# Kernel optimization log

Measured on AMD Instinct MI355X. Metric: run time of the kernel, lower is better.

Reference implementation:

```python
import jax, jax.numpy as jnp
import numpy as np

S, B, E, D, H, F, L = 1024, 8, 768, 8, 8, 2048, 4
D = 1024  # HIDDEN_DIM
H = 8     # nhead
DH = D // H
EPS = 1e-5


def _ln(x, g, b):
    m = jnp.mean(x, -1, keepdims=True)
    v = jnp.mean(jnp.square(x - m), -1, keepdims=True)
    return (x - m) * jax.lax.rsqrt(v + EPS) * g + b


def setup_inputs() -> dict:
    key = jax.random.key(0)
    ks = iter(jax.random.split(key, 16))
    n = lambda shape: jax.random.normal(next(ks), shape, jnp.float32) * 0.02
    return dict(
        x=jax.random.normal(next(ks), (S, B, E), jnp.float32),
        enc_w=n((D, E)), enc_b=jnp.zeros((D,), jnp.float32),
        enc_ln_g=jnp.ones((D,), jnp.float32), enc_ln_b=jnp.zeros((D,), jnp.float32),
        qkv_w=n((L, 3 * D, D)), qkv_b=jnp.zeros((L, 3 * D), jnp.float32),
        out_w=n((L, D, D)), out_b=jnp.zeros((L, D), jnp.float32),
        ln1_g=jnp.ones((L, D), jnp.float32), ln1_b=jnp.zeros((L, D), jnp.float32),
        ff1_w=n((L, F, D)), ff1_b=jnp.zeros((L, F), jnp.float32),
        ff2_w=n((L, D, F)), ff2_b=jnp.zeros((L, D), jnp.float32),
        ln2_g=jnp.ones((L, D), jnp.float32), ln2_b=jnp.zeros((L, D), jnp.float32),
        dec_w1=n((D // 2, D)), dec_b1=jnp.zeros((D // 2,), jnp.float32),
        dec_ln_g=jnp.ones((D // 2,), jnp.float32), dec_ln_b=jnp.zeros((D // 2,), jnp.float32),
        dec_w2=n((E, D // 2)), dec_b2=jnp.zeros((E,), jnp.float32),
    )


def reference(x, enc_w, enc_b, enc_ln_g, enc_ln_b, qkv_w, qkv_b, out_w, out_b,
              ln1_g, ln1_b, ff1_w, ff1_b, ff2_w, ff2_b, ln2_g, ln2_b,
              dec_w1, dec_b1, dec_ln_g, dec_ln_b, dec_w2, dec_b2):
    # encoder MLP: Linear -> LayerNorm -> ReLU (dropout = identity at eval)
    h = jax.nn.relu(_ln(x @ enc_w.T + enc_b, enc_ln_g, enc_ln_b))  # (S,B,D)
    scale = np.float32(1.0 / np.sqrt(DH))
    for l in range(L):  # 4 post-norm TransformerEncoderLayers, eager attention
        qkv = h @ qkv_w[l].T + qkv_b[l]                    # (S,B,3D)
        q, k, v = jnp.split(qkv, 3, axis=-1)
        q = q.reshape(S, B, H, DH)
        k = k.reshape(S, B, H, DH)
        v = v.reshape(S, B, H, DH)
        scores = jnp.einsum('sbhd,tbhd->bhst', q, k) * scale  # (B,H,S,S)
        p = jax.nn.softmax(scores, axis=-1)
        o = jnp.einsum('bhst,tbhd->sbhd', p, v).reshape(S, B, D)
        o = o @ out_w[l].T + out_b[l]
        h = _ln(h + o, ln1_g[l], ln1_b[l])
        f = jax.nn.relu(h @ ff1_w[l].T + ff1_b[l]) @ ff2_w[l].T + ff2_b[l]
        h = _ln(h + f, ln2_g[l], ln2_b[l])
    # decoder MLP
    d = jax.nn.relu(_ln(h @ dec_w1.T + dec_b1, dec_ln_g, dec_ln_b))
    return d @ dec_w2.T + dec_b2  # (S,B,E)
```

## Files before the change

kernel.cpp:

```cpp
#include <hip/hip_runtime.h>
#include <math.h>

#define S_ 1024
#define B_ 8
#define E_ 768
#define D_ 1024
#define H_ 8
#define F_ 2048
#define L_ 4
#define M_ (S_*B_)

typedef unsigned short u16;
typedef unsigned int u32;
typedef u16 u16x8 __attribute__((ext_vector_type(8)));
typedef u16 u16x4 __attribute__((ext_vector_type(4)));
typedef u16 u16x2 __attribute__((ext_vector_type(2)));
typedef u32 u32x2 __attribute__((ext_vector_type(2)));
typedef short bf16x8 __attribute__((ext_vector_type(8)));
typedef float f32x4 __attribute__((ext_vector_type(4)));

#define AS1 __attribute__((address_space(1)))
#define AS3 __attribute__((address_space(3)))

#define QSCALE 0.127517432f

__device__ __forceinline__ void gload_lds16(const void* g, void* l) {
  __builtin_amdgcn_global_load_lds((const AS1 void*)g, (AS3 void*)l, 16, 0, 0);
}
__device__ __forceinline__ u16 f2bf(float f) {
  unsigned u = __builtin_bit_cast(unsigned, f);
  return (u16)((u + 0x7fffu + ((u >> 16) & 1u)) >> 16);
}
__device__ __forceinline__ float bf2f(u16 h) {
  unsigned u = ((unsigned)h) << 16;
  return __builtin_bit_cast(float, u);
}
__device__ __forceinline__ u32 cvtpk(float a, float b) {
  u32 r;
  asm("v_cvt_pk_bf16_f32 %0, %1, %2" : "=v"(r) : "v"(a), "v"(b));
  return r;
}

__global__ __launch_bounds__(256) void conv4(
    const float* __restrict__ s0, u16* __restrict__ d0, int n0,
    const float* __restrict__ s1, u16* __restrict__ d1, int n1,
    const float* __restrict__ s2, u16* __restrict__ d2, int n2,
    const float* __restrict__ s3, u16* __restrict__ d3, int n3)
{
  int total = (n0 + n1 + n2 + n3) >> 2;
  for (int i = blockIdx.x * 256 + threadIdx.x; i < total; i += gridDim.x * 256) {
    int e = i << 2;
    const float* s; u16* d; int off;
    if (e < n0)           { s = s0; d = d0; off = e; }
    else if (e < n0+n1)   { s = s1; d = d1; off = e - n0; }
    else if (e < n0+n1+n2){ s = s2; d = d2; off = e - n0 - n1; }
    else                  { s = s3; d = d3; off = e - n0 - n1 - n2; }
    float4 v = *(const float4*)&s[off];
    u16x4 o; o[0]=f2bf(v.x); o[1]=f2bf(v.y); o[2]=f2bf(v.z); o[3]=f2bf(v.w);
    *(u16x4*)&d[off] = o;
  }
}

template<int ACT, int OUTBF, int SCQ>
__global__ __launch_bounds__(512) void gemm256(
    const u16* __restrict__ A, const u16* __restrict__ W,
    const float* __restrict__ bias, void* __restrict__ Cout,
    int M, int N, int K)
{
  __shared__ u16 lds[73728];
  const int gx = gridDim.x, nwg = gx * gridDim.y;
  const int lin = blockIdx.y * gx + blockIdx.x;
  const int work = (lin & 7) * (nwg >> 3) + (lin >> 3);
  const int bm = (work / gx) * 256, bn = (work % gx) * 128;
  const int tid = threadIdx.x;
  const int l = tid & 63;
  const int w = tid >> 6;
  const int l15 = l & 15, lg = l >> 4;
  const int wr = w >> 2, wc = w & 3;
  const int srow = tid >> 3;
  const int scb  = tid & 7;

  f32x4 acc[8][2] = {};
  const int nt = K >> 6;

#define STAGE(c, k0)                                                        \
  {                                                                         \
    u16* Ab = lds + (c)*24576;                                              \
    u16* Bb = Ab + 16384;                                                   \
    _Pragma("unroll")                                                       \
    for (int u = 0; u < 4; ++u) {                                           \
      int row = u*64 + srow;                                                \
      int cb  = scb ^ (row & 7);                                            \
      gload_lds16(A + (size_t)(bm + row) * K + (k0) + cb*8,                 \
                  Ab + u*4096 + tid*8);                                     \
    }                                                                       \
    _Pragma("unroll")                                                       \
    for (int u = 0; u < 2; ++u) {                                           \
      int row = u*64 + srow;                                                \
      int cb  = scb ^ (row & 7);                                            \
      gload_lds16(W + (size_t)(bn + row) * K + (k0) + cb*8,                 \
                  Bb + u*4096 + tid*8);                                     \
    }                                                                       \
  }

  STAGE(0, 0);
  STAGE(1, 64);
  asm volatile("s_waitcnt vmcnt(6)" ::: "memory");
  __builtin_amdgcn_s_barrier();

  int cr = 0, cw = 2;
  for (int t = 0; t < nt; ++t) {
    if (t + 2 < nt) STAGE(cw, (t + 2) << 6);
    const u16* Ab = lds + cr*24576;
    const u16* Bb = Ab + 16384;
    #pragma unroll
    for (int ks = 0; ks < 2; ++ks) {
      bf16x8 af[8], bf_[2];
      #pragma unroll
      for (int mi = 0; mi < 8; ++mi) {
        int row = wr*128 + mi*16 + l15;
        af[mi] = *(const bf16x8*)&Ab[row*64 + ((ks*4 + lg) ^ (row & 7))*8];
      }
      #pragma unroll
      for (int ni = 0; ni < 2; ++ni) {
        int row = wc*32 + ni*16 + l15;
        bf_[ni] = *(const bf16x8*)&Bb[row*64 + ((ks*4 + lg) ^ (row & 7))*8];
      }
      #pragma unroll
      for (int mi = 0; mi < 8; ++mi)
        #pragma unroll
        for (int ni = 0; ni < 2; ++ni)
          acc[mi][ni] = __builtin_amdgcn_mfma_f32_16x16x32_bf16(af[mi], bf_[ni], acc[mi][ni], 0, 0, 0);
    }
    if (t + 1 < nt) {
      if (t + 2 < nt) { asm volatile("s_waitcnt vmcnt(6)" ::: "memory"); }
      else            { asm volatile("s_waitcnt vmcnt(0)" ::: "memory"); }
      __builtin_amdgcn_s_barrier();
    }
    cr = (cr == 2) ? 0 : cr + 1;
    cw = (cw == 2) ? 0 : cw + 1;
  }
#undef STAGE

  u16* Cb = (u16*)Cout; float* Cf = (float*)Cout;
  #pragma unroll
  for (int ni = 0; ni < 2; ++ni) {
    int col = bn + wc*32 + ni*16 + l15;
    float bv = bias[col];
    #pragma unroll
    for (int mi = 0; mi < 8; ++mi) {
      #pragma unroll
      for (int rr = 0; rr < 4; ++rr) {
        int row = bm + wr*128 + mi*16 + lg*4 + rr;
        float v = acc[mi][ni][rr] + bv;
        if (ACT) v = fmaxf(v, 0.f);
        if (SCQ) { if (col < 1024) v *= QSCALE; }
        if (OUTBF) Cb[(size_t)row * N + col] = f2bf(v);
        else       Cf[(size_t)row * N + col] = v;
      }
    }
  }
}

template<int ACT, int OUTBF, int SCQ>
__global__ __launch_bounds__(256) void gemm_mfma(
    const u16* __restrict__ A, const u16* __restrict__ W,
    const float* __restrict__ bias, void* __restrict__ Cout,
    int M, int N, int K)
{
  __shared__ u16 As[128*32];
  __shared__ u16 Bs[128*32];
  const int gx = gridDim.x, nwg = gx * gridDim.y;
  const int lin = blockIdx.y * gx + blockIdx.x;
  const int work = (lin & 7) * (nwg >> 3) + (lin >> 3);
  const int bm = (work / gx) * 128, bn = (work % gx) * 128;
  const int tid = threadIdx.x;
  const int w = tid >> 6, l = tid & 63;
  const int l15 = l & 15, lg = l >> 4;
  const int wr = w >> 1, wc = w & 1;
  f32x4 acc[4][4] = {};

  for (int k0 = 0; k0 < K; k0 += 32) {
    __syncthreads();
    #pragma unroll
    for (int j = 0; j < 2; ++j) {
      int e = (w*2 + j) * 512 + l * 8;
      int row = e >> 5, ko = (l & 3) * 8;
      gload_lds16(A + (size_t)(bm + row) * K + k0 + ko, &As[(w*2 + j) * 512]);
      gload_lds16(W + (size_t)(bn + row) * K + k0 + ko, &Bs[(w*2 + j) * 512]);
    }
    __syncthreads();
    bf16x8 af[4], bf_[4];
    #pragma unroll
    for (int mi = 0; mi < 4; ++mi) {
      int row = wr*64 + mi*16 + l15;
      af[mi] = *(const bf16x8*)&As[row*32 + lg*8];
    }
    #pragma unroll
    for (int ni = 0; ni < 4; ++ni) {
      int row = wc*64 + ni*16 + l15;
      bf_[ni] = *(const bf16x8*)&Bs[row*32 + lg*8];
    }
    #pragma unroll
    for (int mi = 0; mi < 4; ++mi)
      #pragma unroll
      for (int ni = 0; ni < 4; ++ni)
        acc[mi][ni] = __builtin_amdgcn_mfma_f32_16x16x32_bf16(af[mi], bf_[ni], acc[mi][ni], 0, 0, 0);
  }

  u16* Cb = (u16*)Cout; float* Cf = (float*)Cout;
  #pragma unroll
  for (int ni = 0; ni < 4; ++ni) {
    int col = bn + wc*64 + ni*16 + l15;
    float bv = bias[col];
    #pragma unroll
    for (int mi = 0; mi < 4; ++mi) {
      #pragma unroll
      for (int rr = 0; rr < 4; ++rr) {
        int row = bm + wr*64 + mi*16 + lg*4 + rr;
        float v = acc[mi][ni][rr] + bv;
        if (ACT) v = fmaxf(v, 0.f);
        if (SCQ) { if (col < 1024) v *= QSCALE; }
        if (OUTBF) Cb[(size_t)row * N + col] = f2bf(v);
        else       Cf[(size_t)row * N + col] = v;
      }
    }
  }
}

template<int NV, bool RESID, bool RELU>
__global__ __launch_bounds__(256) void ln_bf16(
    const u16* __restrict__ X, const u16* __restrict__ R,
    const float* __restrict__ g, const float* __restrict__ b,
    u16* __restrict__ Y)
{
  constexpr int D = NV * 256;
  __shared__ float sbuf[8];
  const int tid = threadIdx.x;
  const size_t base = (size_t)blockIdx.x * D + tid * NV;
  float v[NV];
  if constexpr (NV == 4) {
    u16x4 xv = *(const u16x4*)&X[base];
    #pragma unroll
    for (int i = 0; i < 4; ++i) v[i] = bf2f(xv[i]);
    if (RESID) {
      u16x4 rv = *(const u16x4*)&R[base];
      #pragma unroll
      for (int i = 0; i < 4; ++i) v[i] += bf2f(rv[i]);
    }
  } else {
    u16x2 xv = *(const u16x2*)&X[base];
    #pragma unroll
    for (int i = 0; i < 2; ++i) v[i] = bf2f(xv[i]);
    if (RESID) {
      u16x2 rv = *(const u16x2*)&R[base];
      #pragma unroll
      for (int i = 0; i < 2; ++i) v[i] += bf2f(rv[i]);
    }
  }
  float sum = 0.f, sq = 0.f;
  #pragma unroll
  for (int i = 0; i < NV; ++i) { sum += v[i]; sq += v[i]*v[i]; }
  #pragma unroll
  for (int off = 32; off > 0; off >>= 1) {
    sum += __shfl_down(sum, off);
    sq  += __shfl_down(sq, off);
  }
  if ((tid & 63) == 0) { sbuf[tid >> 6] = sum; sbuf[4 + (tid >> 6)] = sq; }
  __syncthreads();
  sum = sbuf[0] + sbuf[1] + sbuf[2] + sbuf[3];
  sq  = sbuf[4] + sbuf[5] + sbuf[6] + sbuf[7];
  const float mean = sum / (float)D;
  const float rstd = rsqrtf(sq / (float)D - mean*mean + 1e-5f);
  const int c0 = tid * NV;
  if constexpr (NV == 4) {
    u16x4 o;
    #pragma unroll
    for (int i = 0; i < 4; ++i) {
      float t = (v[i] - mean) * rstd * g[c0+i] + b[c0+i];
      if (RELU) t = fmaxf(t, 0.f);
      o[i] = f2bf(t);
    }
    *(u16x4*)&Y[base] = o;
  } else {
    u16x2 o;
    #pragma unroll
    for (int i = 0; i < 2; ++i) {
      float t = (v[i] - mean) * rstd * g[c0+i] + b[c0+i];
      if (RELU) t = fmaxf(t, 0.f);
      o[i] = f2bf(t);
    }
    *(u16x2*)&Y[base] = o;
  }
}

__global__ __launch_bounds__(256) void vtrans(
    const u16* __restrict__ QKV, u16* __restrict__ Vt)
{
  __shared__ u16 Ls[32*132];
  const int st = blockIdx.x, bh = blockIdx.y;
  const int bb = bh >> 3, hh = bh & 7;
  const int t = threadIdx.x;
  #pragma unroll
  for (int i = 0; i < 2; ++i) {
    int e = i*256 + t;
    int s = e >> 4, d0 = (e & 15) * 8;
    u16x8 v = *(const u16x8*)&QKV[(size_t)((st*32 + s)*8 + bb)*3072 + 2048 + hh*128 + d0];
    #pragma unroll
    for (int j = 0; j < 4; ++j) {
      u16x2 p; p[0] = v[2*j]; p[1] = v[2*j+1];
      *(u16x2*)&Ls[s*132 + d0 + 2*j] = p;
    }
  }
  __syncthreads();
  #pragma unroll
  for (int i = 0; i < 2; ++i) {
    int e = i*256 + t;
    int d = e >> 2, s0 = (e & 3) * 8;
    u16x8 v;
    #pragma unroll
    for (int j = 0; j < 8; ++j) v[j] = Ls[(s0+j)*132 + d];
    *(u16x8*)&Vt[(size_t)bh*131072 + (size_t)d*1024 + st*32 + s0] = v;
  }
}

__global__ __launch_bounds__(512, 4) void attn_mfma(
    const u16* __restrict__ QKV, const u16* __restrict__ Vt,
    u16* __restrict__ AO)
{
  __shared__ u16 Ks[2][64*128];
  __shared__ u16 Vs[2][128*64];
  __shared__ u16 Pl[8][16*64];
  const int bid = blockIdx.x;
  const int wg = (bid & 7) * 64 + (bid >> 3);
  const int qt = wg & 7, bh = wg >> 3;
  const int bb = bh >> 3, hh = bh & 7;
  const int tid = threadIdx.x, w = tid >> 6, l = tid & 63;
  const int l15 = l & 15, lg = l >> 4;

  bf16x8 aq[4];
  {
    int q = qt*128 + w*16 + l15;
    const u16* qp = QKV + (size_t)(q*8 + bb)*3072 + hh*128 + lg*8;
    #pragma unroll
    for (int kc = 0; kc < 4; ++kc)
      aq[kc] = *(const bf16x8*)(qp + kc*32);
  }
  const u16* vbase = Vt + (size_t)bh*131072;

#define STAGE_KV(c, kt)                                                     \
  {                                                                         \
    _Pragma("unroll")                                                       \
    for (int i = 0; i < 2; ++i) {                                           \
      int e = (w*2 + i) * 512 + l * 8;                                      \
      int krow = e >> 7, d0 = e & 127;                                      \
      int dsw = d0 ^ ((krow & 7) << 3);                                     \
      gload_lds16(QKV + (size_t)(((kt)*64 + krow)*8 + bb)*3072 + 1024       \
                      + hh*128 + dsw,                                       \
                  &Ks[c][(w*2 + i) * 512]);                                 \
      int vd = e >> 6, vc = e & 63;                                         \
      int vsw = vc ^ ((vd & 7) << 3);                                       \
      gload_lds16(vbase + (size_t)vd*1024 + (kt)*64 + vsw,                  \
                  &Vs[c][(w*2 + i) * 512]);                                 \
    }                                                                       \
  }

  f32x4 of[8] = {};
  float mreg = -INFINITY, lpart = 0.f;
  const int psw = (l15 & 7) << 3;

  STAGE_KV(0, 0);
  __syncthreads();

  for (int kt = 0; kt < 16; ++kt) {
    const int cur = kt & 1;
    if (kt + 1 < 16) STAGE_KV(cur ^ 1, kt + 1);

    f32x4 sf[4] = {};
    #pragma unroll
    for (int kc = 0; kc < 4; ++kc) {
      #pragma unroll
      for (int f = 0; f < 4; ++f) {
        int krow = f*16 + l15;
        bf16x8 bk = *(const bf16x8*)&Ks[cur][krow*128 + ((kc*32 + lg*8) ^ ((krow & 7) << 3))];
        sf[f] = __builtin_amdgcn_mfma_f32_16x16x32_bf16(bk, aq[kc], sf[f], 0, 0, 0);
      }
    }

    float pm01 = fmaxf(fmaxf(sf[0][0], sf[0][1]), fmaxf(sf[0][2], sf[0][3]));
    float pm23 = fmaxf(fmaxf(sf[1][0], sf[1][1]), fmaxf(sf[1][2], sf[1][3]));
    float pm45 = fmaxf(fmaxf(sf[2][0], sf[2][1]), fmaxf(sf[2][2], sf[2][3]));
    float pm67 = fmaxf(fmaxf(sf[3][0], sf[3][1]), fmaxf(sf[3][2], sf[3][3]));
    float pmax = fmaxf(fmaxf(pm01, pm23), fmaxf(pm45, pm67));
    pmax = fmaxf(pmax, __shfl_xor(pmax, 16));
    pmax = fmaxf(pmax, __shfl_xor(pmax, 32));

    if (__any(pmax > mreg + 8.f)) {
      float mn = fmaxf(mreg, pmax);
      float al = exp2f(mreg - mn);
      mreg = mn;
      lpart *= al;
      #pragma unroll
      for (int r = 0; r < 4; ++r) {
        float alq = __shfl(al, (l & 48) + lg*4 + r);
        #pragma unroll
        for (int ni = 0; ni < 8; ++ni) of[ni][r] *= alq;
      }
    }

    float psum = 0.f;
    #pragma unroll
    for (int f = 0; f < 4; ++f) {
      float p0 = exp2f(sf[f][0] - mreg);
      float p1 = exp2f(sf[f][1] - mreg);
      float p2 = exp2f(sf[f][2] - mreg);
      float p3 = exp2f(sf[f][3] - mreg);
      psum += (p0 + p1) + (p2 + p3);
      u32x2 pk; pk[0] = cvtpk(p0, p1); pk[1] = cvtpk(p2, p3);
      *(u32x2*)&Pl[w][l15*64 + ((f*16 + lg*4) ^ psw)] = pk;
    }
    lpart += psum;

    bf16x8 pa0 = *(const bf16x8*)&Pl[w][l15*64 + ((lg*8) ^ psw)];
    bf16x8 pa1 = *(const bf16x8*)&Pl[w][l15*64 + ((32 + lg*8) ^ psw)];
    #pragma unroll
    for (int ni = 0; ni < 8; ++ni) {
      int n = ni*16 + l15;
      int nsw = (n & 7) << 3;
      bf16x8 vb0 = *(const bf16x8*)&Vs[cur][n*64 + ((lg*8) ^ nsw)];
      bf16x8 vb1 = *(const bf16x8*)&Vs[cur][n*64 + ((32 + lg*8) ^ nsw)];
      of[ni] = __builtin_amdgcn_mfma_f32_16x16x32_bf16(pa0, vb0, of[ni], 0, 0, 0);
      of[ni] = __builtin_amdgcn_mfma_f32_16x16x32_bf16(pa1, vb1, of[ni], 0, 0, 0);
    }

    if (kt + 1 < 16) __syncthreads();
  }
#undef STAGE_KV

  float ls = lpart;
  ls += __shfl_xor(ls, 16);
  ls += __shfl_xor(ls, 32);
  float inv = 1.f / ls;
  #pragma unroll
  for (int r = 0; r < 4; ++r) {
    float invq = __shfl(inv, (l & 48) + lg*4 + r);
    int q = qt*128 + w*16 + lg*4 + r;
    size_t base = (size_t)(q*8 + bb) * 1024 + hh*128;
    #pragma unroll
    for (int ni = 0; ni < 8; ++ni)
      AO[base + ni*16 + l15] = f2bf(of[ni][r] * invq);
  }
}

#define O_WENC  0ull
#define O_WDEC1 786432ull
#define O_WDEC2 1310720ull
#define O_WLQ   1703936ull
#define O_WLO   4849664ull
#define O_WLF1  5898240ull
#define O_WLF2  7995392ull
#define O_R     10092544ull
#define O_H     35258368ull
#define O_AO    43646976ull
#define O_VT    52035584ull

extern "C" void kernel_launch(void* const* d_in, const int* in_sizes, int n_in,
                              void* d_out, int out_size, void* d_ws, size_t ws_size,
                              hipStream_t stream) {
  (void)in_sizes; (void)n_in; (void)out_size; (void)ws_size;
  const float* x        = (const float*)d_in[0];
  const float* enc_w    = (const float*)d_in[1];
  const float* enc_b    = (const float*)d_in[2];
  const float* enc_ln_g = (const float*)d_in[3];
  const float* enc_ln_b = (const float*)d_in[4];
  const float* qkv_w    = (const float*)d_in[5];
  const float* qkv_b    = (const float*)d_in[6];
  const float* out_w    = (const float*)d_in[7];
  const float* out_b    = (const float*)d_in[8];
  const float* ln1_g    = (const float*)d_in[9];
  const float* ln1_b    = (const float*)d_in[10];
  const float* ff1_w    = (const float*)d_in[11];
  const float* ff1_b    = (const float*)d_in[12];
  const float* ff2_w    = (const float*)d_in[13];
  const float* ff2_b    = (const float*)d_in[14];
  const float* ln2_g    = (const float*)d_in[15];
  const float* ln2_b    = (const float*)d_in[16];
  const float* dec_w1   = (const float*)d_in[17];
  const float* dec_b1   = (const float*)d_in[18];
  const float* dec_ln_g = (const float*)d_in[19];
  const float* dec_ln_b = (const float*)d_in[20];
  const float* dec_w2   = (const float*)d_in[21];
  const float* dec_b2   = (const float*)d_in[22];

  u16* ws16 = (u16*)d_ws;
  u16* wenc  = ws16 + O_WENC;
  u16* wdec1 = ws16 + O_WDEC1;
  u16* wdec2 = ws16 + O_WDEC2;
  u16* wlq   = ws16 + O_WLQ;
  u16* wlo   = ws16 + O_WLO;
  u16* wlf1  = ws16 + O_WLF1;
  u16* wlf2  = ws16 + O_WLF2;
  u16* qkv   = ws16 + O_R;
  u16* bufY  = ws16 + O_R;
  u16* bufG  = ws16 + O_R + 8388608ull;
  u16* xb    = bufG;
  u16* dech  = bufG;
  u16* h     = ws16 + O_H;
  u16* ao    = ws16 + O_AO;
  u16* vt    = ws16 + O_VT;

  const dim3 blk(256);
  const dim3 blk5(512);

  conv4<<<1024, blk, 0, stream>>>(x, xb, 8192*768,
                                  enc_w, wenc, 1024*768,
                                  dec_w1, wdec1, 512*1024,
                                  dec_w2, wdec2, 768*512);
  gemm_mfma<0,1,0><<<dim3(8,64), blk, 0, stream>>>(xb, wenc, enc_b, bufY, M_, 1024, 768);
  ln_bf16<4,false,true><<<M_, blk, 0, stream>>>(bufY, nullptr, enc_ln_g, enc_ln_b, h);

  for (int l = 0; l < L_; ++l) {
    conv4<<<1024, blk, 0, stream>>>(qkv_w + (size_t)l*3145728, wlq, 3145728,
                                    out_w + (size_t)l*1048576, wlo, 1048576,
                                    ff1_w + (size_t)l*2097152, wlf1, 2097152,
                                    ff2_w + (size_t)l*2097152, wlf2, 2097152);
    gemm256<0,1,1><<<dim3(24,32), blk5, 0, stream>>>(h, wlq, qkv_b + (size_t)l*3072, qkv, M_, 3072, 1024);
    vtrans<<<dim3(32,64), blk, 0, stream>>>(qkv, vt);
    attn_mfma<<<512, blk5, 0, stream>>>(qkv, vt, ao);
    gemm256<0,1,0><<<dim3(8,32), blk5, 0, stream>>>(ao, wlo, out_b + (size_t)l*1024, bufY, M_, 1024, 1024);
    ln_bf16<4,true,false><<<M_, blk, 0, stream>>>(bufY, h, ln1_g + (size_t)l*1024, ln1_b + (size_t)l*1024, h);
    gemm256<1,1,0><<<dim3(16,32), blk5, 0, stream>>>(h, wlf1, ff1_b + (size_t)l*2048, bufG, M_, 2048, 1024);
    gemm256<0,1,0><<<dim3(8,32), blk5, 0, stream>>>(bufG, wlf2, ff2_b + (size_t)l*1024, bufY, M_, 1024, 2048);
    ln_bf16<4,true,false><<<M_, blk, 0, stream>>>(bufY, h, ln2_g + (size_t)l*1024, ln2_b + (size_t)l*1024, h);
  }

  gemm_mfma<0,1,0><<<dim3(4,64), blk, 0, stream>>>(h, wdec1, dec_b1, bufY, M_, 512, 1024);
  ln_bf16<2,false,true><<<M_, blk, 0, stream>>>(bufY, nullptr, dec_ln_g, dec_ln_b, dech);
  gemm_mfma<0,0,0><<<dim3(6,64), blk, 0, stream>>>(dech, wdec2, dec_b2, d_out, M_, 768, 512);
}
```

Baseline: 1.064 ms.

## Split GEMM main loop into two ping-pong phases interleaving loads with MFMA

Restructures the bf16 GEMM inner loop into two half-tile phases. Each phase loads half of the A fragments from LDS, issues part of the next stage's global-to-LDS copies, then runs MFMAs under raised wave priority between barriers. This halves the live A-fragment registers and spreads memory issue across the iteration so loads overlap with matrix math. The cost is extra barriers per iteration, which can serialize waves if the phases do not line up.

```diff
diff --git a/kernel.cpp b/kernel.cpp
--- a/kernel.cpp
+++ b/kernel.cpp
@@ -83,16 +83,26 @@
   f32x4 acc[8][2] = {};
   const int nt = K >> 6;
 
-#define STAGE(c, k0)                                                        \
+#define STAGE_A3(c, k0)                                                     \
   {                                                                         \
     u16* Ab = lds + (c)*24576;                                              \
-    u16* Bb = Ab + 16384;                                                   \
     _Pragma("unroll")                                                       \
-    for (int u = 0; u < 4; ++u) {                                           \
+    for (int u = 0; u < 3; ++u) {                                           \
       int row = u*64 + srow;                                                \
       int cb  = scb ^ (row & 7);                                            \
       gload_lds16(A + (size_t)(bm + row) * K + (k0) + cb*8,                 \
                   Ab + u*4096 + tid*8);                                     \
+    }                                                                       \
+  }
+#define STAGE_B3(c, k0)                                                     \
+  {                                                                         \
+    u16* Ab = lds + (c)*24576;                                              \
+    u16* Bb = Ab + 16384;                                                   \
+    {                                                                       \
+      int row = 192 + srow;                                                 \
+      int cb  = scb ^ (row & 7);                                            \
+      gload_lds16(A + (size_t)(bm + row) * K + (k0) + cb*8,                 \
+                  Ab + 12288 + tid*8);                                      \
     }                                                                       \
     _Pragma("unroll")                                                       \
     for (int u = 0; u < 2; ++u) {                                           \
@@ -103,44 +113,73 @@
     }                                                                       \
   }
 
-  STAGE(0, 0);
-  STAGE(1, 64);
+  STAGE_A3(0, 0);  STAGE_B3(0, 0);
+  STAGE_A3(1, 64); STAGE_B3(1, 64);
   asm volatile("s_waitcnt vmcnt(6)" ::: "memory");
   __builtin_amdgcn_s_barrier();
 
   int cr = 0, cw = 2;
   for (int t = 0; t < nt; ++t) {
-    if (t + 2 < nt) STAGE(cw, (t + 2) << 6);
     const u16* Ab = lds + cr*24576;
     const u16* Bb = Ab + 16384;
-    #pragma unroll
-    for (int ks = 0; ks < 2; ++ks) {
-      bf16x8 af[8], bf_[2];
-      #pragma unroll
-      for (int mi = 0; mi < 8; ++mi) {
-        int row = wr*128 + mi*16 + l15;
-        af[mi] = *(const bf16x8*)&Ab[row*64 + ((ks*4 + lg) ^ (row & 7))*8];
-      }
-      #pragma unroll
-      for (int ni = 0; ni < 2; ++ni) {
-        int row = wc*32 + ni*16 + l15;
-        bf_[ni] = *(const bf16x8*)&Bb[row*64 + ((ks*4 + lg) ^ (row & 7))*8];
-      }
-      #pragma unroll
-      for (int mi = 0; mi < 8; ++mi)
+    bf16x8 bf_[2][2];
+    bf16x8 af[4][2];
+
+    #pragma unroll
+    for (int ni = 0; ni < 2; ++ni) {
+      int row = wc*32 + ni*16 + l15;
+      bf_[ni][0] = *(const bf16x8*)&Bb[row*64 + ((lg) ^ (row & 7))*8];
+      bf_[ni][1] = *(const bf16x8*)&Bb[row*64 + ((4 + lg) ^ (row & 7))*8];
+    }
+    #pragma unroll
+    for (int mi = 0; mi < 4; ++mi) {
+      int row = wr*128 + mi*16 + l15;
+      af[mi][0] = *(const bf16x8*)&Ab[row*64 + ((lg) ^ (row & 7))*8];
+      af[mi][1] = *(const bf16x8*)&Ab[row*64 + ((4 + lg) ^ (row & 7))*8];
+    }
+    if (t + 2 < nt) STAGE_A3(cw, (t + 2) << 6);
+    __builtin_amdgcn_s_barrier();
+    asm volatile("s_waitcnt lgkmcnt(0)" ::: "memory");
+    __builtin_amdgcn_sched_barrier(0);
+    __builtin_amdgcn_s_setprio(1);
+    #pragma unroll
+    for (int ks = 0; ks < 2; ++ks)
+      #pragma unroll
+      for (int mi = 0; mi < 4; ++mi)
         #pragma unroll
         for (int ni = 0; ni < 2; ++ni)
-          acc[mi][ni] = __builtin_amdgcn_mfma_f32_16x16x32_bf16(af[mi], bf_[ni], acc[mi][ni], 0, 0, 0);
-    }
-    if (t + 1 < nt) {
-      if (t + 2 < nt) { asm volatile("s_waitcnt vmcnt(6)" ::: "memory"); }
-      else            { asm volatile("s_waitcnt vmcnt(0)" ::: "memory"); }
-      __builtin_amdgcn_s_barrier();
-    }
+          acc[mi][ni] = __builtin_amdgcn_mfma_f32_16x16x32_bf16(af[mi][ks], bf_[ni][ks], acc[mi][ni], 0, 0, 0);
+    __builtin_amdgcn_s_setprio(0);
+    __builtin_amdgcn_s_barrier();
+
+    #pragma unroll
+    for (int mi = 0; mi < 4; ++mi) {
+      int row = wr*128 + (4 + mi)*16 + l15;
+      af[mi][0] = *(const bf16x8*)&Ab[row*64 + ((lg) ^ (row & 7))*8];
+      af[mi][1] = *(const bf16x8*)&Ab[row*64 + ((4 + lg) ^ (row & 7))*8];
+    }
+    if (t + 2 < nt) STAGE_B3(cw, (t + 2) << 6);
+    if (t + 2 < nt)      { asm volatile("s_waitcnt vmcnt(6)" ::: "memory"); }
+    else if (t + 1 < nt) { asm volatile("s_waitcnt vmcnt(0)" ::: "memory"); }
+    __builtin_amdgcn_s_barrier();
+    asm volatile("s_waitcnt lgkmcnt(0)" ::: "memory");
+    __builtin_amdgcn_sched_barrier(0);
+    __builtin_amdgcn_s_setprio(1);
+    #pragma unroll
+    for (int ks = 0; ks < 2; ++ks)
+      #pragma unroll
+      for (int mi = 0; mi < 4; ++mi)
+        #pragma unroll
+        for (int ni = 0; ni < 2; ++ni)
+          acc[4 + mi][ni] = __builtin_amdgcn_mfma_f32_16x16x32_bf16(af[mi][ks], bf_[ni][ks], acc[4 + mi][ni], 0, 0, 0);
+    __builtin_amdgcn_s_setprio(0);
+    __builtin_amdgcn_s_barrier();
+
     cr = (cr == 2) ? 0 : cr + 1;
     cw = (cw == 2) ? 0 : cw + 1;
   }
-#undef STAGE
+#undef STAGE_A3
+#undef STAGE_B3
 
   u16* Cb = (u16*)Cout; float* Cf = (float*)Cout;
   #pragma unroll
```

After: 1.079 ms. No clear change (+1.4%).
